# Kernel optimization log

Hardware: AMD Instinct MI355X
Metric: run time of the kernel (lower is better)

## Reference

```python
import jax, jax.numpy as jnp
import numpy as np

N = 4096            # number of graph nodes (keypoints)
L_MAX = 6
Q = 2
D, H, W = 64, 128, 128
ST = 0.15           # sigma_transition
SP = 0.3            # sigma_pairwise
AU = 1.0            # alpha_unary
L = len(range(0, 2 * L_MAX + 1, Q)) ** 3   # 343 displacement labels


def setup_inputs() -> dict:
    key = jax.random.key(0)
    k1, k2 = jax.random.split(key)
    unary = jax.random.normal(k1, (N, L), dtype=jnp.float32)
    u = jax.random.uniform(k2, (N, N), dtype=jnp.float32)
    dist = (u + u.T) * 0.5  # symmetric pairwise distance matrix
    # Buffer A exactly as in __init__: displacement grid -> RBF transition kernel
    r = np.arange(0, 2 * L_MAX + 1, Q, dtype=np.float32)
    g = np.stack(np.meshgrid(r, r, r, indexing='ij'), axis=3).reshape(-1, 3) - L_MAX
    disp = g[:, ::-1] * 2.0 / np.array([W - 1, H - 1, D - 1], dtype=np.float32)
    A = np.exp(-((disp[:, None, :] - disp[None, :, :]) ** 2).sum(-1) / (2.0 * ST ** 2))
    return {"unary": unary, "dist": dist, "A": jnp.asarray(A, dtype=jnp.float32)}


def _forward(unary, dist, A):
    n, l = unary.shape
    unary = AU * unary
    pairwise = jnp.exp(-dist / (2.0 * SP ** 2))
    INF = jnp.float32(1e30)
    idx = jnp.arange(n)
    d = dist.at[idx, idx].set(INF)  # no self edges

    # ---- Prim's MST rooted at node 0 (addition order = parents-before-children) ----
    in_tree0 = jnp.zeros((n,), dtype=bool).at[0].set(True)
    best0 = d[0]                      # cheapest edge from each node into the tree
    parent0 = jnp.zeros((n,), jnp.int32)
    order0 = jnp.zeros((n,), jnp.int32)

    def prim_body(i, st):
        in_tree, best, parent, order = st
        nxt = jnp.argmin(jnp.where(in_tree, INF, best)).astype(jnp.int32)
        in_tree = in_tree.at[nxt].set(True)
        order = order.at[i].set(nxt)
        upd = (d[nxt] < best) & ~in_tree
        parent = jnp.where(upd, nxt, parent)
        best = jnp.where(upd, d[nxt], best)
        return (in_tree, best, parent, order)

    _, _, parent, order = jax.lax.fori_loop(1, n, prim_body, (in_tree0, best0, parent0, order0))
    root = order[0]  # == 0

    # ---- Upward (leaves -> root) max-sum Viterbi messages along tree edges ----
    ptr0 = jnp.zeros((n, l), jnp.int32)

    def up(carry, c):
        belief, ptr = carry
        p = parent[c]
        # scores[l_c, l_p] = belief[c, l_c] + pairwise(c,p) * A[l_c, l_p]
        scores = belief[c][:, None] + pairwise[c, p] * A
        msg = scores.max(axis=0)                                   # [L]
        ptr = ptr.at[c].set(jnp.argmax(scores, axis=0).astype(jnp.int32))
        belief = belief.at[p].add(jnp.where(c == root, 0.0, msg))  # root sends nothing
        return (belief, ptr), None

    (belief, ptr), _ = jax.lax.scan(up, (unary, ptr0), order[::-1])

    # ---- Downward backtracking (root -> leaves) ----
    def down(labels, c):
        lab = jnp.where(c == root,
                        jnp.argmax(belief[root]).astype(jnp.int32),
                        ptr[c, labels[parent[c]]])
        return labels.at[c].set(lab), None

    labels, _ = jax.lax.scan(down, jnp.zeros((n,), jnp.int32), order)

    # disp_out = -1 everywhere, +1 at selected label, scaled by 1e5
    onehot = jax.nn.one_hot(labels, l, dtype=unary.dtype)
    return (2.0 * onehot - 1.0) * 100000.0


def reference(unary, dist, A):
    return _forward(unary, dist, A)
```

## Files before the change

kernel.cpp:

```cpp
#include <hip/hip_runtime.h>
#include <hip/hip_cooperative_groups.h>
#include <math.h>

namespace cg = cooperative_groups;
typedef unsigned long long u64;

#define NN 4096
#define LBL 343
#define PSTRIDE 344
#define APITCH 344
#define U64MAX 0xFFFFFFFFFFFFFFFFull
#define MST_ROUNDS 12

__global__ void mrf_init_kernel(const float* __restrict__ A, float* __restrict__ Apad,
                                int* __restrict__ compA,
                                u64* __restrict__ minEa, u64* __restrict__ minEb,
                                int* __restrict__ counters)
{
  const int id = blockIdx.x * 256 + threadIdx.x;
  if (id < NN) { compA[id] = id; minEa[id] = U64MAX; minEb[id] = U64MAX; }
  if (id == 0) { counters[0] = NN; counters[1] = NN; counters[2] = 0; }
  if (id < LBL * APITCH) {
    const int r = id / APITCH;
    const int c = id - r * APITCH;
    Apad[id] = (c < LBL) ? A[r * LBL + c] : 0.0f;
  }
}

__global__ __launch_bounds__(1024) void mrf_scan_kernel(
    const float* __restrict__ dist, const int* __restrict__ compR,
    u64* __restrict__ minE, int* __restrict__ counters, int round)
{
  __shared__ int s_cc[16];
  __shared__ u64 s_cv[16];

  if (blockIdx.x == 0 && threadIdx.x == 0) counters[round & 1] = 0;
  if (round > 0 && counters[(round - 1) & 1] <= 1) return;

  const int i    = (blockIdx.x * 1024 + threadIdx.x) >> 6;
  const int lane = threadIdx.x & 63;
  const int wib  = threadIdx.x >> 6;

  const int ci = compR[i];
  const float4* rowp = (const float4*)(dist + (size_t)i * NN);
  const int4* cp = (const int4*)compR;
  u64 best = U64MAX;
  #pragma unroll 4
  for (int k = 0; k < 16; ++k) {
    const int q = k * 64 + lane;
    const float4 dv = rowp[q];
    const int4 cv = cp[q];
    const int j0 = q * 4;
    if (cv.x != ci) { const u64 p = ((u64)__float_as_uint(dv.x) << 24) | ((u64)i << 12) | (u64)(j0    ); best = best < p ? best : p; }
    if (cv.y != ci) { const u64 p = ((u64)__float_as_uint(dv.y) << 24) | ((u64)i << 12) | (u64)(j0 + 1); best = best < p ? best : p; }
    if (cv.z != ci) { const u64 p = ((u64)__float_as_uint(dv.z) << 24) | ((u64)i << 12) | (u64)(j0 + 2); best = best < p ? best : p; }
    if (cv.w != ci) { const u64 p = ((u64)__float_as_uint(dv.w) << 24) | ((u64)i << 12) | (u64)(j0 + 3); best = best < p ? best : p; }
  }
  #pragma unroll
  for (int sh = 32; sh >= 1; sh >>= 1) {
    const u64 o = __shfl_down(best, sh);
    best = best < o ? best : o;
  }
  if (lane == 0) {
    s_cc[wib] = (best == U64MAX) ? -1 : ci;
    s_cv[wib] = best;
  }
  __syncthreads();
  if (threadIdx.x == 0) {
    for (int a = 0; a < 16; ++a) {
      const int c = s_cc[a];
      if (c < 0) continue;
      bool dup = false;
      for (int b2 = 0; b2 < a; ++b2) if (s_cc[b2] == c) { dup = true; break; }
      if (dup) continue;
      u64 b = s_cv[a];
      for (int b2 = a + 1; b2 < 16; ++b2)
        if (s_cc[b2] == c && s_cv[b2] < b) b = s_cv[b2];
      atomicMin(&minE[c & (NN - 1)], b);
    }
  }
}

__global__ __launch_bounds__(1024) void mrf_hook_kernel(
    const int* __restrict__ compR, int* __restrict__ compW,
    const u64* __restrict__ minE, u64* __restrict__ minEnext,
    int* __restrict__ eu, int* __restrict__ ev, unsigned* __restrict__ ew,
    int* __restrict__ counters, int round)
{
  if (round > 0 && counters[(round - 1) & 1] <= 1) return;
  const int i = blockIdx.x * 1024 + threadIdx.x;
  if (i >= NN) return;
  minEnext[i] = U64MAX;

  const int r0 = compR[i];
  int cur = r0;
  for (int guard = 0; guard < NN + 2; ++guard) {
    const u64 e = minE[cur];
    if (e == U64MAX) break;
    const int v = (int)(e & 0xFFF);
    const int t = compR[v];
    if (t == cur) break;
    const u64 te = minE[t];
    if (te != U64MAX) {
      const int tv = (int)(te & 0xFFF);
      if (compR[tv] == cur && cur < t) break;
    }
    cur = t;
  }
  compW[i] = cur;
  if (cur == i) atomicAdd(&counters[round & 1], 1);

  if (r0 == i) {
    const u64 e = minE[i];
    if (e != U64MAX) {
      const int v = (int)(e & 0xFFF);
      const int u = (int)((e >> 12) & 0xFFF);
      const unsigned wb = (unsigned)(e >> 24);
      const int t = compR[v];
      bool mutual = false;
      const u64 te = minE[t];
      if (te != U64MAX) {
        const int tv = (int)(te & 0xFFF);
        mutual = (compR[tv] == i);
      }
      if (!(mutual && i < t)) {
        const int slot = atomicAdd(&counters[2], 1);
        if (slot < NN) { eu[slot] = u; ev[slot] = v; ew[slot] = wb; }
      }
    }
  }
}

__device__ __forceinline__ void scan4096(int* arr, int* tmp16, int tid)
{
  __syncthreads();
  const int base = tid * 4;
  const int c0 = arr[base], c1 = arr[base + 1], c2 = arr[base + 2], c3 = arr[base + 3];
  const int lsum = c0 + c1 + c2 + c3;
  const int lane = tid & 63, wid = tid >> 6;
  int incl = lsum;
  #pragma unroll
  for (int o = 1; o < 64; o <<= 1) {
    const int t = __shfl_up(incl, o);
    if (lane >= o) incl += t;
  }
  if (lane == 63) tmp16[wid] = incl;
  __syncthreads();
  if (tid == 0) {
    int run = 0;
    for (int w = 0; w < 16; ++w) { const int t = tmp16[w]; tmp16[w] = run; run += t; }
  }
  __syncthreads();
  const int excl = tmp16[wid] + incl - lsum;
  arr[base]     = excl;
  arr[base + 1] = excl + c0;
  arr[base + 2] = excl + c0 + c1;
  arr[base + 3] = excl + c0 + c1 + c2;
  __syncthreads();
}

__global__ __launch_bounds__(1024) void mrf_root_kernel(
    const float* __restrict__ dist,
    const int* __restrict__ eu, const int* __restrict__ ev, const unsigned* __restrict__ ew,
    int* __restrict__ parent_g, int* __restrict__ childStart, int* __restrict__ childList,
    int* __restrict__ levStart, int* __restrict__ levNodes, int* __restrict__ segList,
    int* __restrict__ meta, float* __restrict__ w_edge,
    u64* __restrict__ adjList, int* __restrict__ ready, int* __restrict__ cursor)
{
  __shared__ int s_deg[NN];
  __shared__ int s_start[NN];
  __shared__ int s_cur[NN];
  __shared__ int s_parent[NN];
  __shared__ unsigned short s_dep[NN];
  __shared__ unsigned short s_fr[2][NN];
  __shared__ int s_tmp16[16];
  __shared__ int s_fcnt, s_nf;

  const int tid = threadIdx.x;

  for (int j = tid; j < NN; j += 1024) ready[j] = 0;
  if (tid == 0) cursor[0] = 0;

  for (int j = tid; j < NN; j += 1024) s_deg[j] = 0;
  __syncthreads();
  for (int e = tid; e < NN - 1; e += 1024) {
    atomicAdd(&s_deg[eu[e] & (NN - 1)], 1);
    atomicAdd(&s_deg[ev[e] & (NN - 1)], 1);
  }
  __syncthreads();
  for (int j = tid; j < NN; j += 1024) s_start[j] = s_deg[j];
  scan4096(s_start, s_tmp16, tid);
  for (int j = tid; j < NN; j += 1024) s_cur[j] = s_start[j];
  __syncthreads();
  for (int e = tid; e < NN - 1; e += 1024) {
    const int u = eu[e] & (NN - 1), v = ev[e] & (NN - 1);
    const u64 wb = (u64)ew[e];
    const int p1 = atomicAdd(&s_cur[u], 1);
    adjList[p1] = (wb << 12) | (u64)v;
    const int p2 = atomicAdd(&s_cur[v], 1);
    adjList[p2] = (wb << 12) | (u64)u;
  }
  __syncthreads();

  for (int j = tid; j < NN; j += 1024) { s_parent[j] = 0; s_dep[j] = 0; }
  if (tid == 0) { s_fcnt = 1; s_nf = 0; s_fr[0][0] = 0; }
  __syncthreads();
  int cur = 0, lev = 0;
  while (true) {
    const int fcnt = s_fcnt;
    if (fcnt == 0) break;
    for (int idx = tid; idx < fcnt; idx += 1024) {
      const int x = s_fr[cur][idx];
      const int st = s_start[x], dg = s_deg[x];
      for (int a = 0; a < dg; ++a) {
        const u64 ent = adjList[st + a];
        const int nb = (int)(ent & 0xFFF);
        if (nb != s_parent[x] || x == 0) {
          s_parent[nb] = x;
          s_dep[nb] = (unsigned short)(lev + 1);
          const int slot = atomicAdd(&s_nf, 1);
          s_fr[1 - cur][slot] = (unsigned short)nb;
        }
      }
    }
    __syncthreads();
    if (tid == 0) { s_fcnt = s_nf; s_nf = 0; }
    ++lev;
    cur ^= 1;
    __syncthreads();
  }
  const int numLev = lev;
  if (tid == 0) { s_parent[0] = 0; meta[0] = numLev; }
  __syncthreads();

  int* s_cs2 = (int*)s_fr;
  for (int j = tid; j < NN; j += 1024) s_cs2[j] = s_deg[j] - (j != 0 ? 1 : 0);
  scan4096(s_cs2, s_tmp16, tid);
  for (int j = tid; j < NN; j += 1024) childStart[j] = s_cs2[j];
  if (tid == 0) childStart[NN] = NN - 1;
  __syncthreads();

  for (int p = tid; p < NN; p += 1024) {
    const int st = s_start[p], dg = s_deg[p], cs = s_cs2[p];
    const int par = s_parent[p];
    u64 buf[16];
    int m = 0;
    for (int a = 0; a < dg; ++a) {
      const u64 ent = adjList[st + a];
      const int nb = (int)(ent & 0xFFF);
      if (p != 0 && nb == par) continue;
      if (m < 16) {
        int q = m;
        while (q > 0 && buf[q - 1] < ent) { buf[q] = buf[q - 1]; --q; }
        buf[q] = ent;
        ++m;
      } else {
        childList[cs + m] = nb;
        ++m;
      }
    }
    const int lim = m < 16 ? m : 16;
    for (int k = 0; k < lim; ++k) childList[cs + k] = (int)(buf[k] & 0xFFF);
  }

  for (int j = tid; j < NN; j += 1024) s_cur[j] = 0;
  __syncthreads();
  for (int j = tid; j < NN; j += 1024) atomicAdd(&s_cur[s_dep[j]], 1);
  scan4096(s_cur, s_tmp16, tid);
  for (int j = tid; j < NN; j += 1024) { levStart[j] = s_cur[j]; s_start[j] = s_cur[j]; }
  if (tid == 0) levStart[NN] = NN;
  __syncthreads();
  for (int j = tid; j < NN; j += 1024) {
    const int pos = atomicAdd(&s_start[s_dep[j]], 1);
    levNodes[pos] = j;
  }
  __syncthreads();

  if (tid == 0) s_nf = 0;
  for (int j = tid; j < NN; j += 1024) s_cur[j] = 0;
  __syncthreads();
  for (int j = tid; j < NN; j += 1024) {
    const int ce = (j == NN - 1) ? (NN - 1) : s_cs2[j + 1];
    int key = -1;
    if (ce - s_cs2[j] == 0) {
      int c = j;
      while (c != 0) {
        const int par = s_parent[c];
        if (childList[s_cs2[par]] != c) break;
        c = par;
      }
      key = s_dep[c];
      atomicAdd(&s_cur[numLev - 1 - key], 1);
      atomicAdd(&s_nf, 1);
    }
    s_deg[j] = key;
  }
  scan4096(s_cur, s_tmp16, tid);
  for (int j = tid; j < NN; j += 1024) s_start[j] = s_cur[j];
  __syncthreads();
  for (int j = tid; j < NN; j += 1024) {
    const int key = s_deg[j];
    if (key >= 0) {
      const int pos = atomicAdd(&s_start[numLev - 1 - key], 1);
      segList[pos] = j;
    }
  }
  if (tid == 0) meta[1] = s_nf;

  for (int j = tid; j < NN; j += 1024) {
    parent_g[j] = s_parent[j];
    w_edge[j] = (j == 0) ? 0.0f
                         : expf(-dist[(size_t)j * NN + s_parent[j]] / 0.18f);
  }
}

__global__ __launch_bounds__(768) void mrf_solve_kernel(
    const float* __restrict__ unary, const float* __restrict__ Apad,
    float* __restrict__ msgbuf, unsigned short* __restrict__ ptrbuf,
    const int* __restrict__ parent, const int* __restrict__ childStart,
    const int* __restrict__ childList, const int* __restrict__ levStart,
    const int* __restrict__ levNodes, const int* __restrict__ segList,
    const float* __restrict__ w_edge,
    int* __restrict__ labels, const int* __restrict__ meta,
    int* __restrict__ ready, int* __restrict__ cursor)
{
  __shared__ float s_b[APITCH];
  __shared__ float s_pv[8][APITCH];
  __shared__ int   s_pi[8][APITCH];
  __shared__ int   s_lab[NN];
  __shared__ int   s_sidx;
  const int tid = threadIdx.x;
  const bool act = (tid < 688);
  const int t = act ? (tid % 86) : 0;
  const int h = act ? (tid / 86) : 0;
  const int lc0 = h * 43;
  const int lc1 = (h == 7) ? LBL : (lc0 + 43);

  int numLev = meta[0];
  if (numLev < 1) numLev = 1;
  if (numLev > NN) numLev = NN;
  int numSegs = meta[1];
  if (numSegs < 1) numSegs = 1;
  if (numSegs > NN) numSegs = NN;

  bool didRoot = false;

  while (!didRoot) {
    if (tid == 0) s_sidx = atomicAdd(cursor, 1);
    __syncthreads();
    const int sidx = s_sidx;
    if (sidx >= numSegs) break;

    int v = segList[sidx] & (NN - 1);
    if (tid < LBL) s_b[tid] = unary[(size_t)v * LBL + tid];
    __syncthreads();

    while (true) {
      if (v == 0) {
        if (tid == 0) {
          float bv = s_b[0]; int bi = 0;
          for (int l = 1; l < LBL; ++l)
            if (s_b[l] > bv) { bv = s_b[l]; bi = l; }
          labels[0] = bi;
          s_lab[0] = bi;
        }
        __syncthreads();
        didRoot = true;
        break;
      }

      if (act) {
        const float w = w_edge[v];
        const float4* __restrict__ Ap4 = (const float4*)Apad;
        float4 a = Ap4[(size_t)lc0 * 86 + t];
        float sb = s_b[lc0];
        float bv0 = __fadd_rn(sb, __fmul_rn(w, a.x));
        float bv1 = __fadd_rn(sb, __fmul_rn(w, a.y));
        float bv2 = __fadd_rn(sb, __fmul_rn(w, a.z));
        float bv3 = __fadd_rn(sb, __fmul_rn(w, a.w));
        int bi0 = lc0, bi1 = lc0, bi2 = lc0, bi3 = lc0;
        #pragma unroll 2
        for (int lc = lc0 + 1; lc < lc1; ++lc) {
          const float4 av = Ap4[(size_t)lc * 86 + t];
          const float sbl = s_b[lc];
          const float s0 = __fadd_rn(sbl, __fmul_rn(w, av.x));
          const float s1 = __fadd_rn(sbl, __fmul_rn(w, av.y));
          const float s2 = __fadd_rn(sbl, __fmul_rn(w, av.z));
          const float s3 = __fadd_rn(sbl, __fmul_rn(w, av.w));
          if (s0 > bv0) { bv0 = s0; bi0 = lc; }
          if (s1 > bv1) { bv1 = s1; bi1 = lc; }
          if (s2 > bv2) { bv2 = s2; bi2 = lc; }
          if (s3 > bv3) { bv3 = s3; bi3 = lc; }
        }
        const int lpb = t * 4;
        s_pv[h][lpb + 0] = bv0; s_pi[h][lpb + 0] = bi0;
        s_pv[h][lpb + 1] = bv1; s_pi[h][lpb + 1] = bi1;
        s_pv[h][lpb + 2] = bv2; s_pi[h][lpb + 2] = bi2;
        s_pv[h][lpb + 3] = bv3; s_pi[h][lpb + 3] = bi3;
      }
      __syncthreads();

      float fbv = 0.0f;
      if (tid < LBL) {
        fbv = s_pv[0][tid];
        int fbi = s_pi[0][tid];
        #pragma unroll
        for (int hh = 1; hh < 8; ++hh) {
          const float pv = s_pv[hh][tid];
          if (pv > fbv) { fbv = pv; fbi = s_pi[hh][tid]; }
        }
        s_pi[0][tid] = fbi;
      }
      __syncthreads();

      if (tid < 172) {
        const unsigned lo = (unsigned)s_pi[0][2 * tid] & 0xFFFFu;
        const unsigned hi = (2 * tid + 1 < LBL)
                              ? ((unsigned)s_pi[0][2 * tid + 1] & 0xFFFFu) : 0u;
        __hip_atomic_store((unsigned*)(ptrbuf + (size_t)v * PSTRIDE + 2 * tid),
                           lo | (hi << 16),
                           __ATOMIC_RELAXED, __HIP_MEMORY_SCOPE_AGENT);
      }

      const int p = parent[v] & (NN - 1);
      const int csp = childStart[p];
      int degp = childStart[p + 1] - csp;
      if (degp < 1) degp = 1;
      if (degp > 64) degp = 64;
      const bool isCarrier = ((childList[csp] & (NN - 1)) == v);

      if (!isCarrier) {
        if (tid < LBL)
          __hip_atomic_store((unsigned*)&msgbuf[(size_t)v * LBL + tid],
                             __float_as_uint(fbv),
                             __ATOMIC_RELAXED, __HIP_MEMORY_SCOPE_AGENT);
        __syncthreads();
        if (tid == 0)
          __hip_atomic_fetch_add(&ready[p], 1,
                                 __ATOMIC_RELEASE, __HIP_MEMORY_SCOPE_AGENT);
        break;
      }

      if (degp > 1 && tid == 0) {
        long long guard = 0;
        while (__hip_atomic_load(&ready[p], __ATOMIC_RELAXED,
                                 __HIP_MEMORY_SCOPE_AGENT) < degp - 1) {
          __builtin_amdgcn_s_sleep(1);
          if (++guard > 30000000LL) break;
        }
      }
      __syncthreads();

      if (tid < LBL) {
        float nb = __fadd_rn(unary[(size_t)p * LBL + tid], fbv);
        for (int k = 1; k < degp; ++k) {
          const int ch = childList[csp + k] & (NN - 1);
          const unsigned um = __hip_atomic_load(
              (const unsigned*)&msgbuf[(size_t)ch * LBL + tid],
              __ATOMIC_RELAXED, __HIP_MEMORY_SCOPE_AGENT);
          nb = __fadd_rn(nb, __uint_as_float(um));
        }
        s_b[tid] = nb;
      }
      v = p;
      __syncthreads();
    }
  }

  if (!didRoot) return;
  __syncthreads();
  for (int lev = 1; lev < numLev; ++lev) {
    int ls = levStart[lev], le = levStart[lev + 1];
    if (ls < 0) ls = 0;
    if (le > NN) le = NN;
    for (int idx = ls + tid; idx < le; idx += 768) {
      const int c = levNodes[idx] & (NN - 1);
      int pl = s_lab[parent[c] & (NN - 1)];
      if (pl < 0) pl = 0;
      if (pl >= LBL) pl = LBL - 1;
      const unsigned pk = __hip_atomic_load(
          (const unsigned*)(ptrbuf + (size_t)c * PSTRIDE + (pl & ~1)),
          __ATOMIC_RELAXED, __HIP_MEMORY_SCOPE_AGENT);
      const int lab = (pl & 1) ? (int)(pk >> 16) : (int)(pk & 0xFFFFu);
      s_lab[c] = lab;
      labels[c] = lab;
    }
    __syncthreads();
  }
}

__global__ void mrf_out_kernel(const int* __restrict__ labels, float* __restrict__ out)
{
  const int id = blockIdx.x * blockDim.x + threadIdx.x;
  if (id >= NN * LBL) return;
  const int c = id / LBL;
  const int l = id - c * LBL;
  out[id] = (l == labels[c]) ? 100000.0f : -100000.0f;
}

extern "C" void kernel_launch(void* const* d_in, const int* in_sizes, int n_in,
                              void* d_out, int out_size, void* d_ws, size_t ws_size,
                              hipStream_t stream)
{
  (void)in_sizes; (void)n_in; (void)out_size; (void)ws_size;
  const float* unary = (const float*)d_in[0];
  const float* dist  = (const float*)d_in[1];
  const float* A     = (const float*)d_in[2];
  float* out = (float*)d_out;

  char* ws = (char*)d_ws;
  size_t off = 0;
  auto take = [&](size_t bytes) -> void* {
    void* p = (void*)(ws + off);
    off += (bytes + 255) & ~(size_t)255;
    return p;
  };
  float* msgbuf = out;
  unsigned short* ptrbuf = (unsigned short*)take((size_t)NN * PSTRIDE * sizeof(unsigned short));
  float*    Apad       = (float*)   take((size_t)LBL * APITCH * sizeof(float));
  int*      compA      = (int*)     take(NN * sizeof(int));
  int*      compB      = (int*)     take(NN * sizeof(int));
  u64*      minEa      = (u64*)     take(NN * sizeof(u64));
  u64*      minEb      = (u64*)     take(NN * sizeof(u64));
  int*      eu         = (int*)     take(NN * sizeof(int));
  int*      ev         = (int*)     take(NN * sizeof(int));
  unsigned* ew         = (unsigned*)take(NN * sizeof(unsigned));
  int*      counters   = (int*)     take(256);
  int*      parent     = (int*)     take(NN * sizeof(int));
  int*      childStart = (int*)     take((NN + 1) * sizeof(int));
  int*      childList  = (int*)     take(NN * sizeof(int));
  int*      levStart   = (int*)     take((NN + 1) * sizeof(int));
  int*      levNodes   = (int*)     take(NN * sizeof(int));
  int*      segList    = (int*)     take(NN * sizeof(int));
  int*      labels     = (int*)     take(NN * sizeof(int));
  int*      meta       = (int*)     take(256);
  float*    w_edge     = (float*)   take(NN * sizeof(float));
  int*      ready      = (int*)     take(NN * sizeof(int));
  int*      cursor     = (int*)     take(256);
  u64*      adjList    = (u64*)     take((size_t)2 * NN * sizeof(u64));

  hipLaunchKernelGGL(mrf_init_kernel, dim3((LBL * APITCH + 255) / 256), dim3(256),
                     0, stream, A, Apad, compA, minEa, minEb, counters);

  for (int r = 0; r < MST_ROUNDS; ++r) {
    const int* compR = (r & 1) ? compB : compA;
    int*       compW = (r & 1) ? compA : compB;
    u64*       mcur  = (r & 1) ? minEb : minEa;
    u64*       mnext = (r & 1) ? minEa : minEb;
    hipLaunchKernelGGL(mrf_scan_kernel, dim3(256), dim3(1024), 0, stream,
                       dist, compR, mcur, counters, r);
    hipLaunchKernelGGL(mrf_hook_kernel, dim3(4), dim3(1024), 0, stream,
                       compR, compW, mcur, mnext, eu, ev, ew, counters, r);
  }

  hipLaunchKernelGGL(mrf_root_kernel, dim3(1), dim3(1024), 0, stream,
                     dist, eu, ev, ew, parent, childStart, childList,
                     levStart, levNodes, segList, meta, w_edge, adjList,
                     ready, cursor);

  {
    void* args[] = {
      (void*)&unary, (void*)&Apad, (void*)&msgbuf, (void*)&ptrbuf,
      (void*)&parent, (void*)&childStart, (void*)&childList,
      (void*)&levStart, (void*)&levNodes, (void*)&segList, (void*)&w_edge,
      (void*)&labels, (void*)&meta, (void*)&ready, (void*)&cursor
    };
    hipLaunchCooperativeKernel((void*)mrf_solve_kernel, dim3(256), dim3(768),
                               args, 0, stream);
  }

  const int total = NN * LBL;
  hipLaunchKernelGGL(mrf_out_kernel, dim3((total + 255) / 256), dim3(256), 0, stream,
                     labels, out);
}
```

Measured before the change: 912.5 us.

## Cache sub-threshold candidate edges to skip full dist scans in later Boruvka rounds

The first Boruvka round, in addition to finding minimum edges, records each row's edges with distance below a fixed threshold into a per-row candidate list. Later rounds scan only those candidates with one thread per row. A row falls back to a serial full-row scan only when no candidate crosses components or the list overflowed. The minimum-edge result stays exact, but the fallback scan is serial per thread and could be slow once components grow large.

After: 1.073 ms. 1.18x slower.

```diff
diff --git a/kernel.cpp b/kernel.cpp
--- a/kernel.cpp
+++ b/kernel.cpp
@@ -11,6 +11,8 @@
 #define APITCH 344
 #define U64MAX 0xFFFFFFFFFFFFFFFFull
 #define MST_ROUNDS 12
+#define TAU 0.05f
+#define CANDCAP 96
 
 __global__ void mrf_init_kernel(const float* __restrict__ A, float* __restrict__ Apad,
                                 int* __restrict__ compA,
@@ -27,34 +29,53 @@
   }
 }
 
-__global__ __launch_bounds__(1024) void mrf_scan_kernel(
+__global__ __launch_bounds__(1024) void mrf_scan0_kernel(
     const float* __restrict__ dist, const int* __restrict__ compR,
-    u64* __restrict__ minE, int* __restrict__ counters, int round)
+    u64* __restrict__ minE, int* __restrict__ counters,
+    u64* __restrict__ cand, int* __restrict__ candCnt)
 {
   __shared__ int s_cc[16];
   __shared__ u64 s_cv[16];
-
-  if (blockIdx.x == 0 && threadIdx.x == 0) counters[round & 1] = 0;
-  if (round > 0 && counters[(round - 1) & 1] <= 1) return;
+  __shared__ int s_cnt[16];
+
+  if (blockIdx.x == 0 && threadIdx.x == 0) counters[0] = 0;
 
   const int i    = (blockIdx.x * 1024 + threadIdx.x) >> 6;
   const int lane = threadIdx.x & 63;
   const int wib  = threadIdx.x >> 6;
+  if (lane == 0) s_cnt[wib] = 0;
+  __syncthreads();
 
   const int ci = compR[i];
   const float4* rowp = (const float4*)(dist + (size_t)i * NN);
   const int4* cp = (const int4*)compR;
   u64 best = U64MAX;
-  #pragma unroll 4
+  #pragma unroll 2
   for (int k = 0; k < 16; ++k) {
     const int q = k * 64 + lane;
     const float4 dv = rowp[q];
     const int4 cv = cp[q];
     const int j0 = q * 4;
-    if (cv.x != ci) { const u64 p = ((u64)__float_as_uint(dv.x) << 24) | ((u64)i << 12) | (u64)(j0    ); best = best < p ? best : p; }
-    if (cv.y != ci) { const u64 p = ((u64)__float_as_uint(dv.y) << 24) | ((u64)i << 12) | (u64)(j0 + 1); best = best < p ? best : p; }
-    if (cv.z != ci) { const u64 p = ((u64)__float_as_uint(dv.z) << 24) | ((u64)i << 12) | (u64)(j0 + 2); best = best < p ? best : p; }
-    if (cv.w != ci) { const u64 p = ((u64)__float_as_uint(dv.w) << 24) | ((u64)i << 12) | (u64)(j0 + 3); best = best < p ? best : p; }
+    if (cv.x != ci) {
+      const u64 p = ((u64)__float_as_uint(dv.x) << 24) | ((u64)i << 12) | (u64)(j0    );
+      best = best < p ? best : p;
+      if (dv.x < TAU) { const int s = atomicAdd(&s_cnt[wib], 1); if (s < CANDCAP) cand[(size_t)i * CANDCAP + s] = p; }
+    }
+    if (cv.y != ci) {
+      const u64 p = ((u64)__float_as_uint(dv.y) << 24) | ((u64)i << 12) | (u64)(j0 + 1);
+      best = best < p ? best : p;
+      if (dv.y < TAU) { const int s = atomicAdd(&s_cnt[wib], 1); if (s < CANDCAP) cand[(size_t)i * CANDCAP + s] = p; }
+    }
+    if (cv.z != ci) {
+      const u64 p = ((u64)__float_as_uint(dv.z) << 24) | ((u64)i << 12) | (u64)(j0 + 2);
+      best = best < p ? best : p;
+      if (dv.z < TAU) { const int s = atomicAdd(&s_cnt[wib], 1); if (s < CANDCAP) cand[(size_t)i * CANDCAP + s] = p; }
+    }
+    if (cv.w != ci) {
+      const u64 p = ((u64)__float_as_uint(dv.w) << 24) | ((u64)i << 12) | (u64)(j0 + 3);
+      best = best < p ? best : p;
+      if (dv.w < TAU) { const int s = atomicAdd(&s_cnt[wib], 1); if (s < CANDCAP) cand[(size_t)i * CANDCAP + s] = p; }
+    }
   }
   #pragma unroll
   for (int sh = 32; sh >= 1; sh >>= 1) {
@@ -64,6 +85,7 @@
   if (lane == 0) {
     s_cc[wib] = (best == U64MAX) ? -1 : ci;
     s_cv[wib] = best;
+    candCnt[i] = s_cnt[wib];
   }
   __syncthreads();
   if (threadIdx.x == 0) {
@@ -79,6 +101,41 @@
       atomicMin(&minE[c & (NN - 1)], b);
     }
   }
+}
+
+__global__ __launch_bounds__(256) void mrf_scanc_kernel(
+    const float* __restrict__ dist, const int* __restrict__ compR,
+    u64* __restrict__ minE, int* __restrict__ counters, int round,
+    const u64* __restrict__ cand, const int* __restrict__ candCnt)
+{
+  if (blockIdx.x == 0 && threadIdx.x == 0) counters[round & 1] = 0;
+  if (counters[(round - 1) & 1] <= 1) return;
+
+  const int i = blockIdx.x * 256 + threadIdx.x;
+  const int ci = compR[i];
+  u64 best = U64MAX;
+  const int n = candCnt[i];
+  if (n <= CANDCAP) {
+    for (int k = 0; k < n; ++k) {
+      const u64 e = cand[(size_t)i * CANDCAP + k];
+      const int j = (int)(e & 0xFFF);
+      if (compR[j] != ci) best = best < e ? best : e;
+    }
+  }
+  if (best == U64MAX) {
+    const float4* rowp = (const float4*)(dist + (size_t)i * NN);
+    const int4* cp = (const int4*)compR;
+    for (int q = 0; q < NN / 4; ++q) {
+      const float4 dv = rowp[q];
+      const int4 cv = cp[q];
+      const int j0 = q * 4;
+      if (cv.x != ci) { const u64 p = ((u64)__float_as_uint(dv.x) << 24) | ((u64)i << 12) | (u64)(j0    ); best = best < p ? best : p; }
+      if (cv.y != ci) { const u64 p = ((u64)__float_as_uint(dv.y) << 24) | ((u64)i << 12) | (u64)(j0 + 1); best = best < p ? best : p; }
+      if (cv.z != ci) { const u64 p = ((u64)__float_as_uint(dv.z) << 24) | ((u64)i << 12) | (u64)(j0 + 2); best = best < p ? best : p; }
+      if (cv.w != ci) { const u64 p = ((u64)__float_as_uint(dv.w) << 24) | ((u64)i << 12) | (u64)(j0 + 3); best = best < p ? best : p; }
+    }
+  }
+  if (best != U64MAX) atomicMin(&minE[ci & (NN - 1)], best);
 }
 
 __global__ __launch_bounds__(1024) void mrf_hook_kernel(
@@ -518,6 +575,8 @@
   float* msgbuf = out;
   unsigned short* ptrbuf = (unsigned short*)take((size_t)NN * PSTRIDE * sizeof(unsigned short));
   float*    Apad       = (float*)   take((size_t)LBL * APITCH * sizeof(float));
+  u64*      cand       = (u64*)     take((size_t)NN * CANDCAP * sizeof(u64));
+  int*      candCnt    = (int*)     take(NN * sizeof(int));
   int*      compA      = (int*)     take(NN * sizeof(int));
   int*      compB      = (int*)     take(NN * sizeof(int));
   u64*      minEa      = (u64*)     take(NN * sizeof(u64));
@@ -542,13 +601,18 @@
   hipLaunchKernelGGL(mrf_init_kernel, dim3((LBL * APITCH + 255) / 256), dim3(256),
                      0, stream, A, Apad, compA, minEa, minEb, counters);
 
-  for (int r = 0; r < MST_ROUNDS; ++r) {
+  hipLaunchKernelGGL(mrf_scan0_kernel, dim3(256), dim3(1024), 0, stream,
+                     dist, compA, minEa, counters, cand, candCnt);
+  hipLaunchKernelGGL(mrf_hook_kernel, dim3(4), dim3(1024), 0, stream,
+                     compA, compB, minEa, minEb, eu, ev, ew, counters, 0);
+
+  for (int r = 1; r < MST_ROUNDS; ++r) {
     const int* compR = (r & 1) ? compB : compA;
     int*       compW = (r & 1) ? compA : compB;
     u64*       mcur  = (r & 1) ? minEb : minEa;
     u64*       mnext = (r & 1) ? minEa : minEb;
-    hipLaunchKernelGGL(mrf_scan_kernel, dim3(256), dim3(1024), 0, stream,
-                       dist, compR, mcur, counters, r);
+    hipLaunchKernelGGL(mrf_scanc_kernel, dim3(16), dim3(256), 0, stream,
+                       dist, compR, mcur, counters, r, cand, candCnt);
     hipLaunchKernelGGL(mrf_hook_kernel, dim3(4), dim3(1024), 0, stream,
                        compR, compW, mcur, mnext, eu, ev, ew, counters, r);
   }
```
